# Performance work log

Hardware: AMD Instinct MI355X
Metric: run time of the kernel (lower is better)

The kernel has to match this reference:

```python
import jax, jax.numpy as jnp
import numpy as np

B, SQ, SKV, D = 4, 4096, 4096, 64

def setup_inputs() -> dict:
    key = jax.random.key(0)
    kq, kk, kv = jax.random.split(key, 3)
    return {
        "q": jax.random.normal(kq, (B, SQ, D), dtype=jnp.float32),
        "k": jax.random.normal(kk, (B, SKV, D), dtype=jnp.float32),
        "v": jax.random.normal(kv, (B, SKV, D), dtype=jnp.float32),
        "inv_scale_factor": 8,
        "is_training": 0,
    }

def reference(q, k, v, inv_scale_factor, is_training):
    # qk = q @ k^T, divided by inv_scale_factor, softmax over keys
    scores = jnp.einsum("bqd,bkd->bqk", q, k) / inv_scale_factor  # [B,SQ,SKV]
    attn = jax.nn.softmax(scores, axis=-1)
    # dropout is deterministic identity (eval mode, is_training=0)
    out = jnp.einsum("bqk,bkd->bqd", attn, v)  # [B,SQ,D]
    # should_apply_residual before loop
    out = out + q
    # 3-iteration chain: residual add + normalization add (+2q), dropout (identity),
    # sigmoid, clamp(0,1)
    for _ in range(3):
        out = out + 2.0 * q
        out = jax.nn.sigmoid(out)
        out = jnp.clip(out, 0.0, 1.0)
    return out
```

## Files before the change

### kernel.cpp

```cpp
#include <hip/hip_runtime.h>

#define SQd 4096
#define SKVd 4096
#define DDIM 64
#define BK 32
#define NG 8
#define NTILES (SKVd / BK)
#define NCHUNK (NTILES / 2)
#define TPG (NTILES / NG)
#define CPG (TPG / 2)
#define KWS_BYTES ((size_t)4 * NTILES * 2048)
#define BROWS 64

typedef float floatx4  __attribute__((ext_vector_type(4)));
typedef float floatx16 __attribute__((ext_vector_type(16)));
typedef int   intx8    __attribute__((ext_vector_type(8)));

template <bool HI>
__device__ inline int pk2(float a, float b, int old) {
    return __builtin_amdgcn_cvt_pk_fp8_f32(a, b, old, HI);
}

__device__ inline intx8 mk8(int4 a, int4 b) {
    intx8 r;
    r[0] = a.x; r[1] = a.y; r[2] = a.z; r[3] = a.w;
    r[4] = b.x; r[5] = b.y; r[6] = b.z; r[7] = b.w;
    return r;
}

struct CombS {
    float Ored[BROWS][4][68];
    float Lred[BROWS][NG];
};

__global__ __launch_bounds__(256)
void prepack_kernel(const float* __restrict__ k, const float* __restrict__ v,
                    char* __restrict__ ws)
{
    __shared__ __align__(16) float Kt[BK][68];
    __shared__ __align__(16) float Vt[BK][68];

    const int blk  = blockIdx.x;
    const int b    = blk >> 7;
    const int tile = blk & (NTILES - 1);
    const int tid  = threadIdx.x;

    const size_t base = ((size_t)b * SKVd + tile * BK) * DDIM;
    {
        const int row = tid >> 3, col = (tid & 7) * 8;
        const float4 k0 = *(const float4*)(k + base + (size_t)row * DDIM + col);
        const float4 k1 = *(const float4*)(k + base + (size_t)row * DDIM + col + 4);
        *(float4*)&Kt[row][col] = k0; *(float4*)&Kt[row][col + 4] = k1;
        const float4 v0 = *(const float4*)(v + base + (size_t)row * DDIM + col);
        const float4 v1 = *(const float4*)(v + base + (size_t)row * DDIM + col + 4);
        *(float4*)&Vt[row][col] = v0; *(float4*)&Vt[row][col + 4] = v1;
    }
    __syncthreads();

    const int lane = tid & 63;
    const int q4   = tid >> 6;
    const int l31  = lane & 31;
    const int u    = lane >> 5;

    {
        const float* s = &Kt[l31][u * 32 + q4 * 8];
        int w0 = pk2<false>(s[0], s[1], 0); w0 = pk2<true>(s[2], s[3], w0);
        int w1 = pk2<false>(s[4], s[5], 0); w1 = pk2<true>(s[6], s[7], w1);
        int2 o2; o2.x = w0; o2.y = w1;
        *(int2*)(ws + (size_t)(b * NTILES + tile) * 2048 + lane * 32 + q4 * 8) = o2;
    }
    {
        const int h  = q4 >> 1;
        const int rh = (q4 & 1) * 8;
        float p[8];
        #pragma unroll
        for (int i = 0; i < 8; ++i) {
            const int r   = rh + i;
            const int key = (r & 3) + 8 * (r >> 2) + 4 * u;
            p[i] = Vt[key][h * 32 + l31];
        }
        int w0 = pk2<false>(p[0], p[1], 0); w0 = pk2<true>(p[2], p[3], w0);
        int w1 = pk2<false>(p[4], p[5], 0); w1 = pk2<true>(p[6], p[7], w1);
        int2 o2; o2.x = w0; o2.y = w1;
        const size_t voff = KWS_BYTES
            + ((size_t)(b * NCHUNK + (tile >> 1)) * 2 + h) * 2048
            + lane * 32 + (tile & 1) * 16 + rh;
        *(int2*)(ws + voff) = o2;
    }
}

__global__ __launch_bounds__(1024, 4)
void fattn_kernel(const float* __restrict__ q, const int* __restrict__ isf_p,
                  const char* __restrict__ kws, const char* __restrict__ vws,
                  float* __restrict__ out)
{
    __shared__ CombS C;

    const int tid  = threadIdx.x;
    const int wv   = tid >> 6;
    const int g    = wv & 7;
    const int qh   = wv >> 3;
    const int lane = tid & 63;
    const int l31  = lane & 31;
    const int u    = lane >> 5;

    const int bidx  = blockIdx.x;
    const int b     = bidx >> 6;
    const int blkq  = (bidx & 63) * BROWS;
    const int qbase = blkq + qh * 32;

    const float scale = 1.44269504088896340736f / (float)(*isf_p);
    const float SINIT = -4.0f * 1.44269504088896340736f;

    intx8 qf;
    {
        const float* qp = q + ((size_t)b * SQd + qbase + l31) * DDIM + u * 32;
        #pragma unroll
        for (int d = 0; d < 8; ++d) {
            const float4 a = *(const float4*)(qp + 4 * d);
            int w = pk2<false>(a.x * scale, a.y * scale, 0);
            w     = pk2<true >(a.z * scale, a.w * scale, w);
            qf[d] = w;
        }
    }

    const char* kg = kws + (size_t)(b * NTILES + g * TPG) * 2048 + lane * 32;
    const char* vg = vws + (size_t)(b * NCHUNK + g * CPG) * 4096 + lane * 32;
    const int cph  = bidx & (CPG - 1);

    floatx16 o0, o1;
    #pragma unroll
    for (int i = 0; i < 16; ++i) { o0[i] = 0.f; o1[i] = 0.f; }
    const floatx16 zc = o0;
    float l_acc = 0.f;

    int4 k0, k1, k2, k3, v0, v1, v2, v3;
    {
        const size_t off = (size_t)(cph & (CPG - 1)) * 4096;
        k0 = *(const int4*)(kg + off);        k1 = *(const int4*)(kg + off + 16);
        k2 = *(const int4*)(kg + off + 2048); k3 = *(const int4*)(kg + off + 2064);
        v0 = *(const int4*)(vg + off);        v1 = *(const int4*)(vg + off + 16);
        v2 = *(const int4*)(vg + off + 2048); v3 = *(const int4*)(vg + off + 2064);
    }

    #pragma unroll 1
    for (int c = 0; c < CPG; ++c) {
        const size_t offn = (size_t)((c + 1 + cph) & (CPG - 1)) * 4096;

        intx8 pa;
        floatx16 s = __builtin_amdgcn_mfma_scale_f32_32x32x64_f8f6f4(
            mk8(k0, k1), qf, zc, 0, 0, 0, 0x7F7F7F7F, 0, 0x7F7F7F7F);

        const int4 nk0 = *(const int4*)(kg + offn);
        const int4 nk1 = *(const int4*)(kg + offn + 16);
        const int4 nk2 = *(const int4*)(kg + offn + 2048);
        const int4 nk3 = *(const int4*)(kg + offn + 2064);

        #pragma unroll
        for (int r = 0; r < 16; ++r) s[r] = __builtin_amdgcn_exp2f(s[r] + SINIT);
        l_acc += ((((s[0] + s[1]) + (s[2] + s[3])) + ((s[4] + s[5]) + (s[6] + s[7])))
               + (((s[8] + s[9]) + (s[10] + s[11])) + ((s[12] + s[13]) + (s[14] + s[15]))));
        #pragma unroll
        for (int d2 = 0; d2 < 4; ++d2) {
            int w = pk2<false>(s[4 * d2], s[4 * d2 + 1], 0);
            pa[d2] = pk2<true>(s[4 * d2 + 2], s[4 * d2 + 3], w);
        }

        floatx16 s2 = __builtin_amdgcn_mfma_scale_f32_32x32x64_f8f6f4(
            mk8(k2, k3), qf, zc, 0, 0, 0, 0x7F7F7F7F, 0, 0x7F7F7F7F);

        const int4 nv0 = *(const int4*)(vg + offn);
        const int4 nv1 = *(const int4*)(vg + offn + 16);
        const int4 nv2 = *(const int4*)(vg + offn + 2048);
        const int4 nv3 = *(const int4*)(vg + offn + 2064);

        #pragma unroll
        for (int r = 0; r < 16; ++r) s2[r] = __builtin_amdgcn_exp2f(s2[r] + SINIT);
        l_acc += ((((s2[0] + s2[1]) + (s2[2] + s2[3])) + ((s2[4] + s2[5]) + (s2[6] + s2[7])))
               + (((s2[8] + s2[9]) + (s2[10] + s2[11])) + ((s2[12] + s2[13]) + (s2[14] + s2[15]))));
        #pragma unroll
        for (int d2 = 0; d2 < 4; ++d2) {
            int w = pk2<false>(s2[4 * d2], s2[4 * d2 + 1], 0);
            pa[4 + d2] = pk2<true>(s2[4 * d2 + 2], s2[4 * d2 + 3], w);
        }

        o0 = __builtin_amdgcn_mfma_scale_f32_32x32x64_f8f6f4(
            pa, mk8(v0, v1), o0, 0, 0, 0, 0x7F7F7F7F, 0, 0x7F7F7F7F);
        o1 = __builtin_amdgcn_mfma_scale_f32_32x32x64_f8f6f4(
            pa, mk8(v2, v3), o1, 0, 0, 0, 0x7F7F7F7F, 0, 0x7F7F7F7F);

        k0 = nk0; k1 = nk1; k2 = nk2; k3 = nk3;
        v0 = nv0; v1 = nv1; v2 = nv2; v3 = nv3;
    }

    l_acc += __shfl_xor(l_acc, 32);
    if (u == 0) C.Lred[qh * 32 + l31][g] = l_acc;

    if (g < 4) {
        #pragma unroll
        for (int r = 0; r < 16; ++r) {
            const int row = qh * 32 + (r & 3) + 8 * (r >> 2) + 4 * u;
            C.Ored[row][g][l31]      = o0[r];
            C.Ored[row][g][32 + l31] = o1[r];
        }
    }
    __syncthreads();
    if (g >= 4) {
        #pragma unroll
        for (int r = 0; r < 16; ++r) {
            const int row = qh * 32 + (r & 3) + 8 * (r >> 2) + 4 * u;
            C.Ored[row][g - 4][l31]      += o0[r];
            C.Ored[row][g - 4][32 + l31] += o1[r];
        }
    }
    __syncthreads();

    {
        const int row = tid >> 4;
        const int d4  = (tid & 15) * 4;
        float l = 0.0f;
        #pragma unroll
        for (int gg = 0; gg < NG; ++gg) l += C.Lred[row][gg];
        const float rl = 1.0f / l;
        float xs[4] = {0.f, 0.f, 0.f, 0.f};
        #pragma unroll
        for (int s = 0; s < 4; ++s) {
            const float4 t4 = *(const float4*)&C.Ored[row][s][d4];
            xs[0] += t4.x; xs[1] += t4.y; xs[2] += t4.z; xs[3] += t4.w;
        }
        const size_t idx = ((size_t)b * SQd + blkq + row) * DDIM + d4;
        const float4 q4v = *(const float4*)(q + idx);
        const float qs[4] = {q4v.x, q4v.y, q4v.z, q4v.w};
        #pragma unroll
        for (int c = 0; c < 4; ++c) {
            float x = xs[c] * rl + qs[c];
            #pragma unroll
            for (int itc = 0; itc < 3; ++itc) {
                x = x + 2.0f * qs[c];
                x = 1.0f / (1.0f + __expf(-x));
                x = fminf(fmaxf(x, 0.0f), 1.0f);
            }
            xs[c] = x;
        }
        const float4 r4 = {xs[0], xs[1], xs[2], xs[3]};
        *(float4*)(out + idx) = r4;
    }
}

extern "C" void kernel_launch(void* const* d_in, const int* in_sizes, int n_in,
                              void* d_out, int out_size, void* d_ws, size_t ws_size,
                              hipStream_t stream) {
    const float* q = (const float*)d_in[0];
    const float* k = (const float*)d_in[1];
    const float* v = (const float*)d_in[2];
    const int* isf = (const int*)d_in[3];
    float* out = (float*)d_out;
    char* ws = (char*)d_ws;

    prepack_kernel<<<dim3(4 * NTILES), dim3(256), 0, stream>>>(k, v, ws);

    const int nblocks = 4 * (SQd / BROWS);
    fattn_kernel<<<dim3(nblocks), dim3(1024), 0, stream>>>(
        q, isf, ws, ws + KWS_BYTES, out);
}
```

Baseline: 89.24 us.

## Stage K/V fp8 chunks through LDS with async global_load_lds shared across query halves

Both query-half waves of a key group used to load the same K and V fragments straight from global memory into registers. Now one half stages the K chunk and the other the V chunk into LDS with async global_load_lds, so each chunk is fetched once per block. The prepack layout becomes 16-byte-per-lane contiguous to match the direct-to-LDS load width. In exchange, each iteration now has two block-wide barriers and a full vmcnt wait. The per-block phase offset (cph) is also dropped, which may concentrate L2 traffic on the same addresses.

```diff
diff --git a/kernel.cpp b/kernel.cpp
--- a/kernel.cpp
+++ b/kernel.cpp
@@ -32,6 +32,10 @@
     float Ored[BROWS][4][68];
     float Lred[BROWS][NG];
 };
+union ShMem {
+    char  stage[NG * 8192];
+    CombS comb;
+};
 
 __global__ __launch_bounds__(256)
 void prepack_kernel(const float* __restrict__ k, const float* __restrict__ v,
@@ -67,7 +71,8 @@
         int w0 = pk2<false>(s[0], s[1], 0); w0 = pk2<true>(s[2], s[3], w0);
         int w1 = pk2<false>(s[4], s[5], 0); w1 = pk2<true>(s[6], s[7], w1);
         int2 o2; o2.x = w0; o2.y = w1;
-        *(int2*)(ws + (size_t)(b * NTILES + tile) * 2048 + lane * 32 + q4 * 8) = o2;
+        *(int2*)(ws + (size_t)(b * NTILES + tile) * 2048
+                 + (q4 >> 1) * 1024 + lane * 16 + (q4 & 1) * 8) = o2;
     }
     {
         const int h  = q4 >> 1;
@@ -84,7 +89,7 @@
         int2 o2; o2.x = w0; o2.y = w1;
         const size_t voff = KWS_BYTES
             + ((size_t)(b * NCHUNK + (tile >> 1)) * 2 + h) * 2048
-            + lane * 32 + (tile & 1) * 16 + rh;
+            + (tile & 1) * 1024 + lane * 16 + rh;
         *(int2*)(ws + voff) = o2;
     }
 }
@@ -94,7 +99,7 @@
                   const char* __restrict__ kws, const char* __restrict__ vws,
                   float* __restrict__ out)
 {
-    __shared__ CombS C;
+    __shared__ __align__(16) ShMem S;
 
     const int tid  = threadIdx.x;
     const int wv   = tid >> 6;
@@ -124,9 +129,27 @@
         }
     }
 
-    const char* kg = kws + (size_t)(b * NTILES + g * TPG) * 2048 + lane * 32;
-    const char* vg = vws + (size_t)(b * NCHUNK + g * CPG) * 4096 + lane * 32;
-    const int cph  = bidx & (CPG - 1);
+    const char* kg = kws + (size_t)(b * NTILES + g * TPG) * 2048 + lane * 16;
+    const char* vg = vws + (size_t)(b * NCHUNK + g * CPG) * 4096 + lane * 16;
+    const int   gB = g * 8192;
+
+    auto stg = [&](const char* src, int dstoff) {
+        __builtin_amdgcn_global_load_lds(
+            (const __attribute__((address_space(1))) void*)(src),
+            (__attribute__((address_space(3))) void*)(S.stage + dstoff),
+            16, 0, 0);
+    };
+    auto stage_chunk = [&](int c) {
+        if (qh == 0) {
+            const char* s = kg + (size_t)c * 4096;
+            stg(s, gB); stg(s + 1024, gB + 1024);
+            stg(s + 2048, gB + 2048); stg(s + 3072, gB + 3072);
+        } else {
+            const char* s = vg + (size_t)c * 4096;
+            stg(s, gB + 4096); stg(s + 1024, gB + 5120);
+            stg(s + 2048, gB + 6144); stg(s + 3072, gB + 7168);
+        }
+    };
 
     floatx16 o0, o1;
     #pragma unroll
@@ -134,74 +157,70 @@
     const floatx16 zc = o0;
     float l_acc = 0.f;
 
-    int4 k0, k1, k2, k3, v0, v1, v2, v3;
-    {
-        const size_t off = (size_t)(cph & (CPG - 1)) * 4096;
-        k0 = *(const int4*)(kg + off);        k1 = *(const int4*)(kg + off + 16);
-        k2 = *(const int4*)(kg + off + 2048); k3 = *(const int4*)(kg + off + 2064);
-        v0 = *(const int4*)(vg + off);        v1 = *(const int4*)(vg + off + 16);
-        v2 = *(const int4*)(vg + off + 2048); v3 = *(const int4*)(vg + off + 2064);
-    }
+    stage_chunk(0);
+    asm volatile("s_waitcnt vmcnt(0)" ::: "memory");
+    __syncthreads();
 
     #pragma unroll 1
     for (int c = 0; c < CPG; ++c) {
-        const size_t offn = (size_t)((c + 1 + cph) & (CPG - 1)) * 4096;
+        const char* gb = S.stage + gB + lane * 16;
+        const int4 f0 = *(const int4*)(gb);
+        const int4 f1 = *(const int4*)(gb + 1024);
+        const int4 f2 = *(const int4*)(gb + 2048);
+        const int4 f3 = *(const int4*)(gb + 3072);
+        const int4 f4 = *(const int4*)(gb + 4096);
+        const int4 f5 = *(const int4*)(gb + 5120);
+        const int4 f6 = *(const int4*)(gb + 6144);
+        const int4 f7 = *(const int4*)(gb + 7168);
+        __syncthreads();
+
+        if (c + 1 < CPG) stage_chunk(c + 1);
 
         intx8 pa;
-        floatx16 s = __builtin_amdgcn_mfma_scale_f32_32x32x64_f8f6f4(
-            mk8(k0, k1), qf, zc, 0, 0, 0, 0x7F7F7F7F, 0, 0x7F7F7F7F);
-
-        const int4 nk0 = *(const int4*)(kg + offn);
-        const int4 nk1 = *(const int4*)(kg + offn + 16);
-        const int4 nk2 = *(const int4*)(kg + offn + 2048);
-        const int4 nk3 = *(const int4*)(kg + offn + 2064);
-
-        #pragma unroll
-        for (int r = 0; r < 16; ++r) s[r] = __builtin_amdgcn_exp2f(s[r] + SINIT);
-        l_acc += ((((s[0] + s[1]) + (s[2] + s[3])) + ((s[4] + s[5]) + (s[6] + s[7])))
-               + (((s[8] + s[9]) + (s[10] + s[11])) + ((s[12] + s[13]) + (s[14] + s[15]))));
-        #pragma unroll
-        for (int d2 = 0; d2 < 4; ++d2) {
-            int w = pk2<false>(s[4 * d2], s[4 * d2 + 1], 0);
-            pa[d2] = pk2<true>(s[4 * d2 + 2], s[4 * d2 + 3], w);
-        }
-
-        floatx16 s2 = __builtin_amdgcn_mfma_scale_f32_32x32x64_f8f6f4(
-            mk8(k2, k3), qf, zc, 0, 0, 0, 0x7F7F7F7F, 0, 0x7F7F7F7F);
-
-        const int4 nv0 = *(const int4*)(vg + offn);
-        const int4 nv1 = *(const int4*)(vg + offn + 16);
-        const int4 nv2 = *(const int4*)(vg + offn + 2048);
-        const int4 nv3 = *(const int4*)(vg + offn + 2064);
-
-        #pragma unroll
-        for (int r = 0; r < 16; ++r) s2[r] = __builtin_amdgcn_exp2f(s2[r] + SINIT);
-        l_acc += ((((s2[0] + s2[1]) + (s2[2] + s2[3])) + ((s2[4] + s2[5]) + (s2[6] + s2[7])))
-               + (((s2[8] + s2[9]) + (s2[10] + s2[11])) + ((s2[12] + s2[13]) + (s2[14] + s2[15]))));
-        #pragma unroll
-        for (int d2 = 0; d2 < 4; ++d2) {
-            int w = pk2<false>(s2[4 * d2], s2[4 * d2 + 1], 0);
-            pa[4 + d2] = pk2<true>(s2[4 * d2 + 2], s2[4 * d2 + 3], w);
-        }
-
+        {
+            floatx16 s = __builtin_amdgcn_mfma_scale_f32_32x32x64_f8f6f4(
+                mk8(f0, f1), qf, zc, 0, 0, 0, 0x7F7F7F7F, 0, 0x7F7F7F7F);
+            #pragma unroll
+            for (int r = 0; r < 16; ++r) s[r] = __builtin_amdgcn_exp2f(s[r] + SINIT);
+            l_acc += ((((s[0] + s[1]) + (s[2] + s[3])) + ((s[4] + s[5]) + (s[6] + s[7])))
+                   + (((s[8] + s[9]) + (s[10] + s[11])) + ((s[12] + s[13]) + (s[14] + s[15]))));
+            #pragma unroll
+            for (int d2 = 0; d2 < 4; ++d2) {
+                int w = pk2<false>(s[4 * d2], s[4 * d2 + 1], 0);
+                pa[d2] = pk2<true>(s[4 * d2 + 2], s[4 * d2 + 3], w);
+            }
+        }
+        {
+            floatx16 s2 = __builtin_amdgcn_mfma_scale_f32_32x32x64_f8f6f4(
+                mk8(f2, f3), qf, zc, 0, 0, 0, 0x7F7F7F7F, 0, 0x7F7F7F7F);
+            #pragma unroll
+            for (int r = 0; r < 16; ++r) s2[r] = __builtin_amdgcn_exp2f(s2[r] + SINIT);
+            l_acc += ((((s2[0] + s2[1]) + (s2[2] + s2[3])) + ((s2[4] + s2[5]) + (s2[6] + s2[7])))
+                   + (((s2[8] + s2[9]) + (s2[10] + s2[11])) + ((s2[12] + s2[13]) + (s2[14] + s2[15]))));
+            #pragma unroll
+            for (int d2 = 0; d2 < 4; ++d2) {
+                int w = pk2<false>(s2[4 * d2], s2[4 * d2 + 1], 0);
+                pa[4 + d2] = pk2<true>(s2[4 * d2 + 2], s2[4 * d2 + 3], w);
+            }
+        }
         o0 = __builtin_amdgcn_mfma_scale_f32_32x32x64_f8f6f4(
-            pa, mk8(v0, v1), o0, 0, 0, 0, 0x7F7F7F7F, 0, 0x7F7F7F7F);
+            pa, mk8(f4, f5), o0, 0, 0, 0, 0x7F7F7F7F, 0, 0x7F7F7F7F);
         o1 = __builtin_amdgcn_mfma_scale_f32_32x32x64_f8f6f4(
-            pa, mk8(v2, v3), o1, 0, 0, 0, 0x7F7F7F7F, 0, 0x7F7F7F7F);
-
-        k0 = nk0; k1 = nk1; k2 = nk2; k3 = nk3;
-        v0 = nv0; v1 = nv1; v2 = nv2; v3 = nv3;
+            pa, mk8(f6, f7), o1, 0, 0, 0, 0x7F7F7F7F, 0, 0x7F7F7F7F);
+
+        asm volatile("s_waitcnt vmcnt(0)" ::: "memory");
+        __syncthreads();
     }
 
     l_acc += __shfl_xor(l_acc, 32);
-    if (u == 0) C.Lred[qh * 32 + l31][g] = l_acc;
+    if (u == 0) S.comb.Lred[qh * 32 + l31][g] = l_acc;
 
     if (g < 4) {
         #pragma unroll
         for (int r = 0; r < 16; ++r) {
             const int row = qh * 32 + (r & 3) + 8 * (r >> 2) + 4 * u;
-            C.Ored[row][g][l31]      = o0[r];
-            C.Ored[row][g][32 + l31] = o1[r];
+            S.comb.Ored[row][g][l31]      = o0[r];
+            S.comb.Ored[row][g][32 + l31] = o1[r];
         }
     }
     __syncthreads();
@@ -209,8 +228,8 @@
         #pragma unroll
         for (int r = 0; r < 16; ++r) {
             const int row = qh * 32 + (r & 3) + 8 * (r >> 2) + 4 * u;
-            C.Ored[row][g - 4][l31]      += o0[r];
-            C.Ored[row][g - 4][32 + l31] += o1[r];
+            S.comb.Ored[row][g - 4][l31]      += o0[r];
+            S.comb.Ored[row][g - 4][32 + l31] += o1[r];
         }
     }
     __syncthreads();
@@ -220,12 +239,12 @@
         const int d4  = (tid & 15) * 4;
         float l = 0.0f;
         #pragma unroll
-        for (int gg = 0; gg < NG; ++gg) l += C.Lred[row][gg];
+        for (int gg = 0; gg < NG; ++gg) l += S.comb.Lred[row][gg];
         const float rl = 1.0f / l;
         float xs[4] = {0.f, 0.f, 0.f, 0.f};
         #pragma unroll
         for (int s = 0; s < 4; ++s) {
-            const float4 t4 = *(const float4*)&C.Ored[row][s][d4];
+            const float4 t4 = *(const float4*)&S.comb.Ored[row][s][d4];
             xs[0] += t4.x; xs[1] += t4.y; xs[2] += t4.z; xs[3] += t4.w;
         }
         const size_t idx = ((size_t)b * SQd + blkq + row) * DDIM + d4;
```

Measured after the change: 93.96 us. 1.05x slower.
